# Performance work log

Hardware: AMD Instinct MI355X
Metric: run time of the kernel (lower is better)

## Reference

```python
import jax, jax.numpy as jnp
import numpy as np
from jax import lax

B, C, H, W = 16, 512, 32, 32
CQ = C // 8  # 64
EPS = 1e-5
NEG_SLOPE = 0.2


def _conv1x1(x, Wm, b):
    # x: [B,C,H,W], Wm: [O,C] (1x1 conv kernel squeezed), b: [O]
    return jnp.einsum('oc,bchw->bohw', Wm, x) + b[None, :, None, None]


def _calc_mean_std(feat):
    b, c = feat.shape[:2]
    v = feat.reshape(b, c, -1)
    mean = v.mean(axis=2)[:, :, None, None]
    var = v.var(axis=2, ddof=1) + EPS  # torch .var is unbiased
    std = jnp.sqrt(var)[:, :, None, None]
    return mean, std


def setup_inputs() -> dict:
    key = jax.random.key(0)
    ks = jax.random.split(key, 8)
    s = 0.02
    return {
        'inp': jax.random.normal(ks[0], (B, C, H, W), jnp.float32),
        'x': jax.random.normal(ks[1], (B, C, H, W), jnp.float32),
        'y': jax.random.normal(ks[2], (B, C, H, W), jnp.float32),
        'Wq': jax.random.normal(ks[3], (CQ, C), jnp.float32) * s,
        'bq': jnp.zeros((CQ,), jnp.float32),
        'Wk': jax.random.normal(ks[4], (CQ, C), jnp.float32) * s,
        'bk': jnp.zeros((CQ,), jnp.float32),
        'Wv': jax.random.normal(ks[5], (C, C), jnp.float32) * s,
        'bv': jnp.zeros((C,), jnp.float32),
        'Wc': jax.random.normal(ks[6], (C, 2 * C, 3, 3), jnp.float32) * s,
        'bc': jnp.zeros((C,), jnp.float32),
        'alpha': jnp.ones((1,), jnp.float32),
        'beta': jnp.ones((1,), jnp.float32),
    }


def reference(inp, x, y, Wq, bq, Wk, bk, Wv, bv, Wc, bc, alpha, beta):
    b, c, h, w = x.shape
    n = h * w
    t = float(CQ) ** 0.5  # default temperature sqrt(c_in//8)

    # --- identity-row attention: query from x, key from y ---
    pq = _conv1x1(x, Wq, bq).reshape(b, CQ, n)   # [b,cq,n]
    pk = _conv1x1(y, Wk, bk).reshape(b, CQ, n)
    pv = _conv1x1(x, Wv, bv).reshape(b, c, n)    # [b,c,n]
    attn_iden = jax.nn.softmax(jnp.einsum('bcn,bcm->bnm', pq, pk) / t, axis=-1)

    # --- pose-row attention: query from y, key from x ---
    pq_p = _conv1x1(y, Wq, bq).reshape(b, CQ, n)
    pk_p = _conv1x1(x, Wk, bk).reshape(b, CQ, n)
    attn_pose = jax.nn.softmax(jnp.einsum('bcn,bcm->bnm', pq_p, pk_p) / t, axis=-1)

    # x_update = bmm(value, attn_iden^T): out[c,m] = sum_n pv[c,n]*attn[m,n]
    x_update = jnp.einsum('bcn,bmn->bcm', pv, attn_iden).reshape(b, c, h, w)
    x_update = (1.0 - beta) * x + beta * x_update

    # --- AdaIN: normalize inp, re-affine with x stats ---
    t_mean, t_std = _calc_mean_std(x)
    i_mean, i_std = _calc_mean_std(inp)
    adained = (inp - i_mean) / i_std * t_std + t_mean

    # reverse attention combine with (1 - attn_pose)
    rev = jnp.einsum('bcn,bmn->bcm', adained.reshape(b, c, n), 1.0 - attn_pose)
    rev = rev.reshape(b, c, h, w)
    rev = (1.0 - alpha) * rev + alpha * adained

    # --- conv_comp: 3x3 conv (2C -> C), same padding, LeakyReLU(0.2) ---
    cat = jnp.concatenate([x_update, rev], axis=1)  # [b,2c,h,w]
    out = lax.conv_general_dilated(
        cat, Wc, window_strides=(1, 1), padding='SAME',
        dimension_numbers=('NCHW', 'OIHW', 'NCHW'))
    out = out + bc[None, :, None, None]
    out = jnp.where(out >= 0, out, NEG_SLOPE * out)
    return out
```

## Files before the change

### kernel.cpp

```cpp
#include <hip/hip_runtime.h>

typedef unsigned short u16;
typedef unsigned int u32;

using bf16x8 = __attribute__((ext_vector_type(8))) __bf16;
using f32x4  = __attribute__((ext_vector_type(4))) float;
using u16x4  = __attribute__((ext_vector_type(4))) unsigned short;

__device__ __forceinline__ f32x4 MFMA(bf16x8 a, bf16x8 b, f32x4 c) {
    return __builtin_amdgcn_mfma_f32_16x16x32_bf16(a, b, c, 0, 0, 0);
}

__device__ __forceinline__ u16 f2bf(float f) {
    u32 u = __builtin_bit_cast(u32, f);
    u = (u + 0x7FFFu + ((u >> 16) & 1u)) >> 16;
    return (u16)u;
}
__device__ __forceinline__ float bf2f(u16 h) {
    return __builtin_bit_cast(float, (u32)h << 16);
}

typedef const __attribute__((address_space(1))) unsigned int* gp_t;
typedef __attribute__((address_space(3))) unsigned int* lp_t;

__device__ __forceinline__ void gload16(const void* g, void* l) {
    __builtin_amdgcn_global_load_lds((gp_t)g, (lp_t)l, 16, 0, 0);
}

#define NPADR  1156

static constexpr size_t OFF_XT   = 0;
static constexpr size_t OFF_YT   = OFF_XT  + (size_t)16*1024*512*2;
static constexpr size_t OFF_PJX  = OFF_YT  + (size_t)16*1024*512*2;
static constexpr size_t OFF_PJY  = OFF_PJX + (size_t)16*1024*128*2;
static constexpr size_t OFF_PV   = OFF_PJY + (size_t)16*1024*128*2;
static constexpr size_t OFF_AD   = OFF_PV  + (size_t)16*512*1024*2;
static constexpr size_t OFF_ATTN = OFF_AD  + (size_t)16*512*1024*2;
static constexpr size_t OFF_ATT2 = OFF_ATTN+ (size_t)16*1024*1024*2;
static constexpr size_t OFF_CATT = OFF_ATT2+ (size_t)16*1024*1024*2;
static constexpr size_t OFF_WQK  = OFF_CATT+ (size_t)16*1156*1024*2;
static constexpr size_t OFF_WV   = OFF_WQK + (size_t)128*512*2;
static constexpr size_t OFF_WT   = OFF_WV  + (size_t)512*512*2;
static constexpr size_t OFF_SA   = OFF_WT  + (size_t)9*512*1024*2;
static constexpr size_t OFF_OA   = OFF_SA  + (size_t)16*512*4;
static constexpr size_t OFF_TM   = OFF_OA  + (size_t)16*512*4;

__global__ __launch_bounds__(256) void k_prep_w(const float* __restrict__ Wq,
                                                const float* __restrict__ Wk,
                                                const float* __restrict__ Wv,
                                                u16* __restrict__ wqk, u16* __restrict__ wv) {
    int i = blockIdx.x * 256 + threadIdx.x;
    if (i < 128 * 512) {
        float v = (i < 64 * 512) ? Wq[i] : Wk[i - 64 * 512];
        wqk[i] = f2bf(v);
    }
    if (i < 512 * 512) wv[i] = f2bf(Wv[i]);
}

__global__ __launch_bounds__(256) void k_prep_wt(const float* __restrict__ Wc, u16* __restrict__ wt) {
    int e = blockIdx.x * 256 + threadIdx.x;
    const float* src = Wc + (size_t)e * 9;
#pragma unroll
    for (int tap = 0; tap < 9; tap++) wt[(size_t)tap * 524288 + e] = f2bf(src[tap]);
}

__global__ __launch_bounds__(256) void k_border(u16* __restrict__ catT) {
    int cell = blockIdx.x, b = blockIdx.y;
    int row, col;
    if (cell < 34)       { row = 0;  col = cell; }
    else if (cell < 68)  { row = 33; col = cell - 34; }
    else if (cell < 100) { row = cell - 68 + 1;  col = 0; }
    else                 { row = cell - 100 + 1; col = 33; }
    u16* dst = catT + ((size_t)b * NPADR + row * 34 + col) * 1024;
    u16x4 z = {0, 0, 0, 0};
    ((u16x4*)dst)[threadIdx.x] = z;
}

__global__ __launch_bounds__(256) void k_stats(const float* __restrict__ x, const float* __restrict__ inp,
                                               u16* __restrict__ ad, float* __restrict__ tmA) {
    int row = blockIdx.x;
    int t = threadIdx.x;
    const float4* xr = (const float4*)(x + (size_t)row * 1024);
    const float4* ir = (const float4*)(inp + (size_t)row * 1024);
    float4 a = xr[t], c = ir[t];
    float s1 = a.x + a.y + a.z + a.w;
    float s2 = a.x * a.x + a.y * a.y + a.z * a.z + a.w * a.w;
    float p1 = c.x + c.y + c.z + c.w;
    float p2 = c.x * c.x + c.y * c.y + c.z * c.z + c.w * c.w;
#pragma unroll
    for (int m = 32; m; m >>= 1) {
        s1 += __shfl_xor(s1, m); s2 += __shfl_xor(s2, m);
        p1 += __shfl_xor(p1, m); p2 += __shfl_xor(p2, m);
    }
    __shared__ float red[4][4];
    __shared__ float bcast[2];
    int wv = t >> 6;
    if ((t & 63) == 0) { red[wv][0] = s1; red[wv][1] = s2; red[wv][2] = p1; red[wv][3] = p2; }
    __syncthreads();
    if (t == 0) {
        s1 = red[0][0] + red[1][0] + red[2][0] + red[3][0];
        s2 = red[0][1] + red[1][1] + red[2][1] + red[3][1];
        p1 = red[0][2] + red[1][2] + red[2][2] + red[3][2];
        p2 = red[0][3] + red[1][3] + red[2][3] + red[3][3];
        float tm = s1 * (1.0f / 1024.0f);
        float ts = sqrtf((s2 - 1024.0f * tm * tm) * (1.0f / 1023.0f) + 1e-5f);
        float im = p1 * (1.0f / 1024.0f);
        float is = sqrtf((p2 - 1024.0f * im * im) * (1.0f / 1023.0f) + 1e-5f);
        float sc = ts / is;
        bcast[0] = sc; bcast[1] = tm - im * sc;
        tmA[row] = tm;
    }
    __syncthreads();
    float sc = bcast[0], of = bcast[1];
    u16x4 r;
    r[0] = f2bf(c.x * sc + of); r[1] = f2bf(c.y * sc + of);
    r[2] = f2bf(c.z * sc + of); r[3] = f2bf(c.w * sc + of);
    ((u16x4*)(ad + (size_t)row * 1024))[t] = r;
}

__global__ __launch_bounds__(256) void k_transpose(const float* __restrict__ x, const float* __restrict__ y,
                                                   u16* __restrict__ xT, u16* __restrict__ yT) {
    __shared__ float tile[64][65];
    int b = blockIdx.y;
    int ct = blockIdx.x >> 4;
    int nt = blockIdx.x & 15;
    const float* src = blockIdx.z ? y : x;
    u16* dst = blockIdx.z ? yT : xT;
    int c0 = ct * 64, n0 = nt * 64;
    int ln = threadIdx.x & 63, wv = threadIdx.x >> 6;
#pragma unroll
    for (int i = 0; i < 16; i++) {
        int cl = wv + i * 4;
        tile[cl][ln] = src[((size_t)(b * 512 + c0 + cl)) * 1024 + n0 + ln];
    }
    __syncthreads();
#pragma unroll
    for (int i = 0; i < 16; i++) {
        int nl = wv + i * 4;
        dst[((size_t)(b * 1024 + n0 + nl)) * 512 + c0 + ln] = f2bf(tile[ln][nl]);
    }
}

template <int KTOT, int LDA, int LDB>
__device__ __forceinline__ void gemm128(const u16* __restrict__ Aorig, const u16* __restrict__ Borig,
                                        f32x4 (&acc)[4][4]) {
    __shared__ __align__(16) u16 lds[32768];
    constexpr int NT = KTOT / 32;
    const int tid = threadIdx.x;
    const int l = tid & 63, w = tid >> 6;
    const int lr = l & 15, lg = l >> 4;
    const int moff = (w >> 1) * 64, coff = (w & 1) * 64;
    char* ldsb = (char*)lds;
    auto stage = [&](const u16* orig, int ldx, int bufByte) {
#pragma unroll
        for (int it = 0; it < 2; it++) {
            int slot = it * 256 + tid;
            gload16(orig + (size_t)(slot & 127) * ldx + (slot >> 7) * 8,
                    ldsb + bufByte + it * 4096 + w * 1024);
        }
    };
    auto stageT = [&](int t, int s) {
        stage(Aorig + t * 32, LDA, s * 8192);
        stage(Borig + t * 32, LDB, 32768 + s * 8192);
    };
    stageT(0, 0);
    stageT(1, 1);
    stageT(2, 2);
#pragma unroll 1
    for (int q = 0; q < NT; q++) {
        int qq = q + 3; if (qq >= NT) qq -= NT;
        stageT(qq, (q + 3) & 3);
        asm volatile("s_waitcnt vmcnt(12)" ::: "memory");
        __builtin_amdgcn_s_barrier();
        const char* A = ldsb + (q & 3) * 8192;
        const char* B = ldsb + 32768 + (q & 3) * 8192;
        bf16x8 af[4], bb[4];
#pragma unroll
        for (int i = 0; i < 4; i++) af[i] = *(const bf16x8*)(A + lg * 2048 + (moff + 16 * i + lr) * 16);
#pragma unroll
        for (int i = 0; i < 4; i++) bb[i] = *(const bf16x8*)(B + lg * 2048 + (coff + 16 * i + lr) * 16);
        __builtin_amdgcn_s_setprio(1);
#pragma unroll
        for (int ri = 0; ri < 4; ri++)
#pragma unroll
            for (int ci = 0; ci < 4; ci++) acc[ri][ci] = MFMA(af[ri], bb[ci], acc[ri][ci]);
        __builtin_amdgcn_s_setprio(0);
        __builtin_amdgcn_s_barrier();
    }
    asm volatile("s_waitcnt vmcnt(0)" ::: "memory");
}

__global__ __launch_bounds__(256) void k_proj(const u16* __restrict__ xT, const u16* __restrict__ yT,
                                              const u16* __restrict__ wqk, const float* __restrict__ bq,
                                              const float* __restrict__ bk, u16* __restrict__ pjx,
                                              u16* __restrict__ pjy) {
    int b = blockIdx.y;
    const u16* S = blockIdx.z ? yT : xT;
    u16* D = blockIdx.z ? pjy : pjx;
    int nb = blockIdx.x * 128;
    f32x4 acc[4][4];
#pragma unroll
    for (int i = 0; i < 4; i++)
#pragma unroll
        for (int j = 0; j < 4; j++) acc[i][j] = f32x4{0.f, 0.f, 0.f, 0.f};
    gemm128<512, 512, 512>(S + ((size_t)b * 1024 + nb) * 512, wqk, acc);
    int l = threadIdx.x & 63, w = threadIdx.x >> 6;
    int lr = l & 15, lg = l >> 4;
    int moff = (w >> 1) * 64, coff = (w & 1) * 64;
#pragma unroll
    for (int ri = 0; ri < 4; ri++) {
#pragma unroll
        for (int r = 0; r < 4; r++) {
            int n = nb + moff + 16 * ri + 4 * lg + r;
#pragma unroll
            for (int ci = 0; ci < 4; ci++) {
                int cq = coff + 16 * ci + lr;
                float bias = (cq < 64) ? bq[cq] : bk[cq - 64];
                D[((size_t)b * 1024 + n) * 128 + cq] = f2bf(acc[ri][ci][r] + bias);
            }
        }
    }
}

__global__ __launch_bounds__(256) void k_pv(const u16* __restrict__ xT, const u16* __restrict__ wv,
                                            const float* __restrict__ bv, u16* __restrict__ pv) {
    int b = blockIdx.z;
    int mb = blockIdx.y * 128;
    int nb = blockIdx.x * 128;
    f32x4 acc[4][4];
#pragma unroll
    for (int i = 0; i < 4; i++)
#pragma unroll
        for (int j = 0; j < 4; j++) acc[i][j] = f32x4{0.f, 0.f, 0.f, 0.f};
    gemm128<512, 512, 512>(wv + (size_t)mb * 512, xT + ((size_t)b * 1024 + nb) * 512, acc);
    int l = threadIdx.x & 63, w = threadIdx.x >> 6;
    int lr = l & 15, lg = l >> 4;
    int moff = (w >> 1) * 64, coff = (w & 1) * 64;
#pragma unroll
    for (int ri = 0; ri < 4; ri++) {
#pragma unroll
        for (int r = 0; r < 4; r++) {
            int co = mb + moff + 16 * ri + 4 * lg + r;
            float bias = bv[co];
#pragma unroll
            for (int ci = 0; ci < 4; ci++) {
                int n = nb + coff + 16 * ci + lr;
                pv[((size_t)b * 512 + co) * 1024 + n] = f2bf(acc[ri][ci][r] + bias);
            }
        }
    }
}

__global__ __launch_bounds__(256) void k_score(const u16* __restrict__ pjx, const u16* __restrict__ pjy,
                                               u16* __restrict__ attnA, u16* __restrict__ attnB) {
    const u16* qT = blockIdx.y ? pjy : pjx;
    const u16* kT = blockIdx.y ? pjx : pjy;
    u16* attn = blockIdx.y ? attnB : attnA;
    int g = blockIdx.x * 4 + (threadIdx.x >> 6);
    int b = g >> 6, rb = g & 63;
    int l = threadIdx.x & 63, lr = l & 15, lg = l >> 4;
    int mb = rb * 16;
    const u16* qbase = qT + ((size_t)b * 1024 + mb + lr) * 128 + lg * 8;
    bf16x8 a0 = *(const bf16x8*)(qbase);
    bf16x8 a1 = *(const bf16x8*)(qbase + 32);
    const u16* kbase = kT + ((size_t)b * 1024 + lr) * 128 + 64 + lg * 8;
    f32x4 zero = {0.f, 0.f, 0.f, 0.f};
    float mrun[4] = {-1e30f, -1e30f, -1e30f, -1e30f};
    float srun[4] = {0.f, 0.f, 0.f, 0.f};
    for (int cf = 0; cf < 64; cf++) {
        bf16x8 b0 = *(const bf16x8*)(kbase + (size_t)cf * 16 * 128);
        bf16x8 b1 = *(const bf16x8*)(kbase + (size_t)cf * 16 * 128 + 32);
        f32x4 acc = zero;
        acc = MFMA(a0, b0, acc);
        acc = MFMA(a1, b1, acc);
#pragma unroll
        for (int r = 0; r < 4; r++) {
            float v = acc[r] * 0.125f;
            float mn = fmaxf(mrun[r], v);
            srun[r] = srun[r] * __expf(mrun[r] - mn) + __expf(v - mn);
            mrun[r] = mn;
        }
    }
#pragma unroll
    for (int m = 1; m < 16; m <<= 1) {
#pragma unroll
        for (int r = 0; r < 4; r++) {
            float mo = __shfl_xor(mrun[r], m);
            float so = __shfl_xor(srun[r], m);
            float mn = fmaxf(mrun[r], mo);
            srun[r] = srun[r] * __expf(mrun[r] - mn) + so * __expf(mo - mn);
            mrun[r] = mn;
        }
    }
    float inv[4];
#pragma unroll
    for (int r = 0; r < 4; r++) inv[r] = 1.0f / srun[r];
    for (int cf = 0; cf < 64; cf++) {
        bf16x8 b0 = *(const bf16x8*)(kbase + (size_t)cf * 16 * 128);
        bf16x8 b1 = *(const bf16x8*)(kbase + (size_t)cf * 16 * 128 + 32);
        f32x4 acc = zero;
        acc = MFMA(a0, b0, acc);
        acc = MFMA(a1, b1, acc);
#pragma unroll
        for (int r = 0; r < 4; r++) {
            float v = __expf(acc[r] * 0.125f - mrun[r]) * inv[r];
            attn[((size_t)b * 1024 + mb + 4 * lg + r) * 1024 + cf * 16 + lr] = f2bf(v);
        }
    }
}

__global__ __launch_bounds__(256) void k_value(const u16* __restrict__ attnA, const u16* __restrict__ attnB,
                                               const u16* __restrict__ pv, const u16* __restrict__ ad,
                                               const u16* __restrict__ xT, const float* __restrict__ tmA,
                                               const float* __restrict__ alpha, const float* __restrict__ beta,
                                               u16* __restrict__ catT) {
    int z = blockIdx.z;
    int b = z & 15, var = z >> 4;
    const u16* attn = var ? attnB : attnA;
    const u16* V = var ? ad : pv;
    int mb = blockIdx.x * 128;
    int cb = blockIdx.y * 128;
    f32x4 acc[4][4];
#pragma unroll
    for (int i = 0; i < 4; i++)
#pragma unroll
        for (int j = 0; j < 4; j++) acc[i][j] = f32x4{0.f, 0.f, 0.f, 0.f};
    gemm128<1024, 1024, 1024>(attn + ((size_t)b * 1024 + mb) * 1024,
                              V + ((size_t)b * 512 + cb) * 1024, acc);
    int l = threadIdx.x & 63, w = threadIdx.x >> 6;
    int lr = l & 15, lg = l >> 4;
    int moff = (w >> 1) * 64, coff = (w & 1) * 64;
    float sc = var ? alpha[0] : beta[0];
#pragma unroll
    for (int ri = 0; ri < 4; ri++) {
#pragma unroll
        for (int r = 0; r < 4; r++) {
            int m = mb + moff + 16 * ri + 4 * lg + r;
            int pidx = ((m >> 5) + 1) * 34 + (m & 31) + 1;
#pragma unroll
            for (int ci = 0; ci < 4; ci++) {
                int c = cb + coff + 16 * ci + lr;
                float av = acc[ri][ci][r];
                float res;
                if (var == 0) {
                    float xv = bf2f(xT[((size_t)b * 1024 + m) * 512 + c]);
                    res = (1.f - sc) * xv + sc * av;
                } else {
                    float tm = tmA[b * 512 + c];
                    float adv = bf2f(ad[((size_t)b * 512 + c) * 1024 + m]);
                    res = (1.f - sc) * (1024.f * tm - av) + sc * adv;
                }
                catT[((size_t)b * NPADR + pidx) * 1024 + (var ? 512 : 0) + c] = f2bf(res);
            }
        }
    }
}

__global__ __launch_bounds__(512, 2) void k_conv(const u16* __restrict__ wt, const u16* __restrict__ catT,
                                                 const float* __restrict__ bc, float* __restrict__ out) {
    extern __shared__ __align__(16) char dyn[];
    const int tid = threadIdx.x;
    const int l = tid & 63, w = tid >> 6;
    const int lr = l & 15, lg = l >> 4;
    const int b = blockIdx.z;
    const int ob = blockIdx.x * 128;
    const int pb = blockIdx.y * 256;
    const int r0 = blockIdx.y * 8;
    const int ow = w >> 2, pw = w & 3;
    const u16* catB = catT + (size_t)b * NPADR * 1024 + (size_t)r0 * 34 * 1024;

    auto stageA = [&](int tap, int ck, int slot) {
        char* base = dyn + slot * 8192;
        int row = tid & 127, g = tid >> 7;
        gload16(wt + ((size_t)tap * 512 + ob + row) * 1024 + ck + g * 8,
                base + g * 2048 + row * 16);
    };
    auto stageB = [&](int ck, int sel) {
        char* base = dyn + 24576 + sel * 24576;
#pragma unroll
        for (int it = 0; it < 3; it++) {
            int idx = it * 512 + tid;
            int g = idx / 384;
            int row = idx - g * 384;
            gload16(catB + (size_t)row * 1024 + ck + g * 8,
                    base + g * 6144 + row * 16);
        }
    };

    int aoff[4], rbase[4];
#pragma unroll
    for (int i = 0; i < 4; i++) {
        aoff[i] = lg * 2048 + (ow * 64 + 16 * i + lr) * 16;
        int p = pw * 64 + 16 * i + lr;
        rbase[i] = ((p >> 5) + 1) * 34 + (p & 31) + 1;
    }

    f32x4 acc[4][4];
#pragma unroll
    for (int i = 0; i < 4; i++)
#pragma unroll
        for (int j = 0; j < 4; j++) acc[i][j] = f32x4{0.f, 0.f, 0.f, 0.f};

    stageA(0, 0, 0);
    stageB(0, 0);
    stageA(1, 0, 1);
    int phase = 0;
#pragma unroll 1
    for (int ckI = 0; ckI < 32; ckI++) {
#pragma unroll
        for (int tap = 0; tap < 9; tap++, phase++) {
            {
                int t2 = tap + 2;
                int c2 = ckI + (t2 >= 9);
                if (t2 >= 9) t2 -= 9;
                if (c2 >= 32) c2 = 0;
                stageA(t2, c2 * 32, (phase + 2) % 3);
            }
            if (tap == 5) {
                int cn = ckI + 1;
                stageB((cn >= 32 ? 0 : cn) * 32, cn & 1);
            }
            if (tap >= 5 && tap <= 7) asm volatile("s_waitcnt vmcnt(5)" ::: "memory");
            else                      asm volatile("s_waitcnt vmcnt(2)" ::: "memory");
            __builtin_amdgcn_s_barrier();
            const char* A = dyn + (phase % 3) * 8192;
            const char* B = dyn + 24576 + (ckI & 1) * 24576;
            const int drow = (tap / 3 - 1) * 34 + (tap % 3 - 1);
            bf16x8 af[4], bb[4];
#pragma unroll
            for (int i = 0; i < 4; i++) af[i] = *(const bf16x8*)(A + aoff[i]);
#pragma unroll
            for (int i = 0; i < 4; i++) bb[i] = *(const bf16x8*)(B + lg * 6144 + (rbase[i] + drow) * 16);
            __builtin_amdgcn_s_setprio(1);
#pragma unroll
            for (int ri = 0; ri < 4; ri++)
#pragma unroll
                for (int ci = 0; ci < 4; ci++) acc[ri][ci] = MFMA(af[ri], bb[ci], acc[ri][ci]);
            __builtin_amdgcn_s_setprio(0);
            __builtin_amdgcn_s_barrier();
        }
    }
    asm volatile("s_waitcnt vmcnt(0)" ::: "memory");
#pragma unroll
    for (int ri = 0; ri < 4; ri++) {
#pragma unroll
        for (int r = 0; r < 4; r++) {
            int o = ob + ow * 64 + 16 * ri + 4 * lg + r;
            float bias = bc[o];
#pragma unroll
            for (int ci = 0; ci < 4; ci++) {
                int p = pb + pw * 64 + 16 * ci + lr;
                float v = acc[ri][ci][r] + bias;
                v = (v >= 0.f) ? v : 0.2f * v;
                out[((size_t)b * 512 + o) * 1024 + p] = v;
            }
        }
    }
}

extern "C" void kernel_launch(void* const* d_in, const int* in_sizes, int n_in,
                              void* d_out, int out_size, void* d_ws, size_t ws_size,
                              hipStream_t stream) {
    (void)in_sizes; (void)n_in; (void)out_size; (void)ws_size;
    const float* inp = (const float*)d_in[0];
    const float* x   = (const float*)d_in[1];
    const float* y   = (const float*)d_in[2];
    const float* Wq  = (const float*)d_in[3];
    const float* bq  = (const float*)d_in[4];
    const float* Wk  = (const float*)d_in[5];
    const float* bk  = (const float*)d_in[6];
    const float* Wv  = (const float*)d_in[7];
    const float* bv  = (const float*)d_in[8];
    const float* Wc  = (const float*)d_in[9];
    const float* bc  = (const float*)d_in[10];
    const float* alpha = (const float*)d_in[11];
    const float* beta  = (const float*)d_in[12];
    float* out = (float*)d_out;

    char* ws = (char*)d_ws;
    u16* xT   = (u16*)(ws + OFF_XT);
    u16* yT   = (u16*)(ws + OFF_YT);
    u16* pjx  = (u16*)(ws + OFF_PJX);
    u16* pjy  = (u16*)(ws + OFF_PJY);
    u16* pv   = (u16*)(ws + OFF_PV);
    u16* ad   = (u16*)(ws + OFF_AD);
    u16* attnA = (u16*)(ws + OFF_ATTN);
    u16* attnB = (u16*)(ws + OFF_ATT2);
    u16* catT = (u16*)(ws + OFF_CATT);
    u16* wqk  = (u16*)(ws + OFF_WQK);
    u16* wv   = (u16*)(ws + OFF_WV);
    u16* wt   = (u16*)(ws + OFF_WT);
    float* tmA = (float*)(ws + OFF_TM);

    hipFuncSetAttribute((const void*)k_conv, hipFuncAttributeMaxDynamicSharedMemorySize, 73728);

    k_prep_w<<<1024, 256, 0, stream>>>(Wq, Wk, Wv, wqk, wv);
    k_prep_wt<<<2048, 256, 0, stream>>>(Wc, wt);
    k_border<<<dim3(132, 16), 256, 0, stream>>>(catT);
    k_stats<<<8192, 256, 0, stream>>>(x, inp, ad, tmA);
    k_transpose<<<dim3(128, 16, 2), 256, 0, stream>>>(x, y, xT, yT);
    k_proj<<<dim3(8, 16, 2), 256, 0, stream>>>(xT, yT, wqk, bq, bk, pjx, pjy);
    k_pv<<<dim3(8, 4, 16), 256, 0, stream>>>(xT, wv, bv, pv);
    k_score<<<dim3(256, 2), 256, 0, stream>>>(pjx, pjy, attnA, attnB);
    k_value<<<dim3(8, 4, 32), 256, 0, stream>>>(attnA, attnB, pv, ad, xT, tmA, alpha, beta, catT);
    k_conv<<<dim3(4, 4, 16), 512, 73728, stream>>>(wt, catT, bc, out);
}
```

Baseline: 406.6 us.

## Retile value GEMM to 256x256 with triple-buffered LDS pipeline and XCD-aware block mapping

Replaces the value-stage GEMM (previously 128x128 tiles via gemm128 with 256 threads) with a 512-thread kernel computing 256x256 tiles, a three-slot shared-memory pipeline staged with async loads, and a setprio around the MFMA burst. Blocks are now launched as a flat grid remapped so that tiles sharing a batch and variant land on the same XCD, and the conv kernel gets the same XCD-aware remapping. The aim is more operand reuse per load, better latency hiding and better L2 locality, at the cost of more registers and LDS per block and only 256 blocks in the value stage.

```diff
diff --git a/kernel.cpp b/kernel.cpp
--- a/kernel.cpp
+++ b/kernel.cpp
@@ -309,37 +309,83 @@
     }
 }
 
-__global__ __launch_bounds__(256) void k_value(const u16* __restrict__ attnA, const u16* __restrict__ attnB,
-                                               const u16* __restrict__ pv, const u16* __restrict__ ad,
-                                               const u16* __restrict__ xT, const float* __restrict__ tmA,
-                                               const float* __restrict__ alpha, const float* __restrict__ beta,
-                                               u16* __restrict__ catT) {
-    int z = blockIdx.z;
-    int b = z & 15, var = z >> 4;
-    const u16* attn = var ? attnB : attnA;
-    const u16* V = var ? ad : pv;
-    int mb = blockIdx.x * 128;
-    int cb = blockIdx.y * 128;
-    f32x4 acc[4][4];
+__global__ __launch_bounds__(512, 2) void k_value(const u16* __restrict__ attnA, const u16* __restrict__ attnB,
+                                                  const u16* __restrict__ pv, const u16* __restrict__ ad,
+                                                  const u16* __restrict__ xT, const float* __restrict__ tmA,
+                                                  const float* __restrict__ alpha, const float* __restrict__ beta,
+                                                  u16* __restrict__ catT) {
+    extern __shared__ __align__(16) char dyn[];
+    const int id = blockIdx.x;
+    const int xcd = id & 7, j = id >> 3;
+    const int z = xcd + 8 * (j & 3);
+    const int tile = j >> 2;
+    const int mbt = tile & 3, cbt = tile >> 2;
+    const int b = z & 15, var = z >> 4;
+    const u16* Aorig = (var ? attnB : attnA) + ((size_t)b * 1024 + mbt * 256) * 1024;
+    const u16* Borig = (var ? ad : pv) + ((size_t)b * 512 + cbt * 256) * 1024;
+
+    const int tid = threadIdx.x;
+    const int l = tid & 63, w = tid >> 6;
+    const int lr = l & 15, lg = l >> 4;
+    const int ow = w >> 1, pw = w & 1;
+
+    auto stageT = [&](int t, int s) {
+        char* base = dyn + s * 32768;
+#pragma unroll
+        for (int it = 0; it < 2; it++) {
+            int idx = it * 512 + tid;
+            int row = idx & 255, g = idx >> 8;
+            gload16(Aorig + (size_t)row * 1024 + t * 32 + g * 8, base + g * 4096 + row * 16);
+        }
+#pragma unroll
+        for (int it = 0; it < 2; it++) {
+            int idx = it * 512 + tid;
+            int row = idx & 255, g = idx >> 8;
+            gload16(Borig + (size_t)row * 1024 + t * 32 + g * 8, base + 16384 + g * 4096 + row * 16);
+        }
+    };
+
+    f32x4 acc[4][8];
 #pragma unroll
     for (int i = 0; i < 4; i++)
 #pragma unroll
-        for (int j = 0; j < 4; j++) acc[i][j] = f32x4{0.f, 0.f, 0.f, 0.f};
-    gemm128<1024, 1024, 1024>(attn + ((size_t)b * 1024 + mb) * 1024,
-                              V + ((size_t)b * 512 + cb) * 1024, acc);
-    int l = threadIdx.x & 63, w = threadIdx.x >> 6;
-    int lr = l & 15, lg = l >> 4;
-    int moff = (w >> 1) * 64, coff = (w & 1) * 64;
+        for (int jj = 0; jj < 8; jj++) acc[i][jj] = f32x4{0.f, 0.f, 0.f, 0.f};
+
+    stageT(0, 0);
+    stageT(1, 1);
+#pragma unroll 1
+    for (int q = 0; q < 32; q++) {
+        int qq = q + 2; if (qq >= 32) qq -= 32;
+        stageT(qq, (q + 2) % 3);
+        asm volatile("s_waitcnt vmcnt(8)" ::: "memory");
+        __builtin_amdgcn_s_barrier();
+        const char* A = dyn + (q % 3) * 32768;
+        const char* B = A + 16384;
+        bf16x8 af[4], bb[8];
+#pragma unroll
+        for (int i = 0; i < 4; i++) af[i] = *(const bf16x8*)(A + lg * 4096 + (ow * 64 + 16 * i + lr) * 16);
+#pragma unroll
+        for (int i = 0; i < 8; i++) bb[i] = *(const bf16x8*)(B + lg * 4096 + (pw * 128 + 16 * i + lr) * 16);
+        __builtin_amdgcn_s_setprio(1);
+#pragma unroll
+        for (int ri = 0; ri < 4; ri++)
+#pragma unroll
+            for (int ci = 0; ci < 8; ci++) acc[ri][ci] = MFMA(af[ri], bb[ci], acc[ri][ci]);
+        __builtin_amdgcn_s_setprio(0);
+        __builtin_amdgcn_s_barrier();
+    }
+    asm volatile("s_waitcnt vmcnt(0)" ::: "memory");
+
     float sc = var ? alpha[0] : beta[0];
 #pragma unroll
     for (int ri = 0; ri < 4; ri++) {
 #pragma unroll
         for (int r = 0; r < 4; r++) {
-            int m = mb + moff + 16 * ri + 4 * lg + r;
+            int m = mbt * 256 + ow * 64 + 16 * ri + 4 * lg + r;
             int pidx = ((m >> 5) + 1) * 34 + (m & 31) + 1;
 #pragma unroll
-            for (int ci = 0; ci < 4; ci++) {
-                int c = cb + coff + 16 * ci + lr;
+            for (int ci = 0; ci < 8; ci++) {
+                int c = cbt * 256 + pw * 128 + 16 * ci + lr;
                 float av = acc[ri][ci][r];
                 float res;
                 if (var == 0) {
@@ -359,13 +405,18 @@
 __global__ __launch_bounds__(512, 2) void k_conv(const u16* __restrict__ wt, const u16* __restrict__ catT,
                                                  const float* __restrict__ bc, float* __restrict__ out) {
     extern __shared__ __align__(16) char dyn[];
+    const int id = blockIdx.x;
+    const int xcd = id & 7, j = id >> 3;
+    const int obt = j & 3;
+    const int pbb = xcd + 8 * (j >> 2);
+    const int pbt = pbb & 3, b = pbb >> 2;
+
     const int tid = threadIdx.x;
     const int l = tid & 63, w = tid >> 6;
     const int lr = l & 15, lg = l >> 4;
-    const int b = blockIdx.z;
-    const int ob = blockIdx.x * 128;
-    const int pb = blockIdx.y * 256;
-    const int r0 = blockIdx.y * 8;
+    const int ob = obt * 128;
+    const int pb = pbt * 256;
+    const int r0 = pbt * 8;
     const int ow = w >> 2, pw = w & 3;
     const u16* catB = catT + (size_t)b * NPADR * 1024 + (size_t)r0 * 34 * 1024;
 
@@ -399,7 +450,7 @@
 #pragma unroll
     for (int i = 0; i < 4; i++)
 #pragma unroll
-        for (int j = 0; j < 4; j++) acc[i][j] = f32x4{0.f, 0.f, 0.f, 0.f};
+        for (int jj = 0; jj < 4; jj++) acc[i][jj] = f32x4{0.f, 0.f, 0.f, 0.f};
 
     stageA(0, 0, 0);
     stageB(0, 0);
@@ -492,7 +543,8 @@
     u16* wt   = (u16*)(ws + OFF_WT);
     float* tmA = (float*)(ws + OFF_TM);
 
-    hipFuncSetAttribute((const void*)k_conv, hipFuncAttributeMaxDynamicSharedMemorySize, 73728);
+    hipFuncSetAttribute((const void*)k_conv,  hipFuncAttributeMaxDynamicSharedMemorySize, 73728);
+    hipFuncSetAttribute((const void*)k_value, hipFuncAttributeMaxDynamicSharedMemorySize, 98304);
 
     k_prep_w<<<1024, 256, 0, stream>>>(Wq, Wk, Wv, wqk, wv);
     k_prep_wt<<<2048, 256, 0, stream>>>(Wc, wt);
@@ -502,6 +554,6 @@
     k_proj<<<dim3(8, 16, 2), 256, 0, stream>>>(xT, yT, wqk, bq, bk, pjx, pjy);
     k_pv<<<dim3(8, 4, 16), 256, 0, stream>>>(xT, wv, bv, pv);
     k_score<<<dim3(256, 2), 256, 0, stream>>>(pjx, pjy, attnA, attnB);
-    k_value<<<dim3(8, 4, 32), 256, 0, stream>>>(attnA, attnB, pv, ad, xT, tmA, alpha, beta, catT);
-    k_conv<<<dim3(4, 4, 16), 512, 73728, stream>>>(wt, catT, bc, out);
-}
+    k_value<<<256, 512, 98304, stream>>>(attnA, attnB, pv, ad, xT, tmA, alpha, beta, catT);
+    k_conv<<<256, 512, 73728, stream>>>(wt, catT, bc, out);
+}
```

After: 378.6 us. 6.9% less time.
